# Kernel tuning notes

Measured on AMD Instinct MI355X. Metric: run time of the kernel, lower is better.

## Reference

```python
import jax, jax.numpy as jnp
import numpy as np

# ---- module hyperparameters (init_kwargs) ----
M = 6          # truncation level
D = 5          # path dimension
C = 4.0        # phi parameter
A = 1.0        # phi parameter a
SIGLEN = (D ** (M + 1) - 1) // (D - 1) - 1  # 19530
B, S = 64, 32  # batch x samples
N_BISECT = 100

# level id (1..M) of each signature coordinate: d^k coords at level k
LEVELS = jnp.asarray(np.repeat(np.arange(1, M + 1), [D ** k for k in range(1, M + 1)]), dtype=jnp.float32)  # [L]
# one-hot [L, M] mapping coordinates to their level, for per-level squared-norm sums
LEVEL_ONEHOT = jnp.asarray((np.repeat(np.arange(1, M + 1), [D ** k for k in range(1, M + 1)])[:, None] == np.arange(1, M + 1)[None, :]).astype(np.float32))


def setup_inputs() -> dict:
    key = jax.random.key(0)
    signatures = jax.random.normal(key, (B, S, SIGLEN), dtype=jnp.float32) * 0.5
    return {"signatures": signatures}


def _phi(x):
    # phi(x) = x for x <= C, else C + C^(1+a) (C^-a - x^-a)/a
    return jnp.where(x > C, C + C ** (1.0 + A) * (C ** (-A) - x ** (-A)) / A, x)


def _dilatation_norm(x):
    """x: [B,S,L] signatures. Returns norm lambda in [0,1], shape [B,S,1].
    Solves c0 + sum_k c_k t^{2k} = 0 on [0,2] by bisection (replaces brentq)."""
    x2 = x * x
    norm_quad = 1.0 + jnp.sum(x2, axis=-1)          # [B,S]
    c0 = 1.0 - _phi(norm_quad)                      # [B,S], <= 0
    ck = jnp.einsum('bsl,lm->bsm', x2, LEVEL_ONEHOT)  # [B,S,M] per-level squared norms
    coeffs = jnp.concatenate([c0[..., None], ck], axis=-1)  # [B,S,M+1]
    ks = jnp.arange(M + 1, dtype=jnp.float32)

    def poly(t):  # t: [B,S]
        return jnp.sum(coeffs * (t[..., None] ** 2) ** ks, axis=-1)

    def body(i, carry):
        lo, hi = carry
        mid = 0.5 * (lo + hi)
        neg = poly(mid) < 0.0
        return jnp.where(neg, mid, lo), jnp.where(neg, hi, mid)

    lo = jnp.zeros_like(c0)
    hi = jnp.full_like(c0, 2.0)
    lo, hi = jax.lax.fori_loop(0, N_BISECT, body, (lo, hi))
    root = 0.5 * (lo + hi)
    root = jnp.where(jnp.all(jnp.isfinite(coeffs), axis=-1), root, 0.0)
    root = jnp.minimum(root, 1.0)  # clamp as in dilatation()
    return root[..., None]          # [B,S,1]


def reference(signatures):
    # Normalization.apply + rescale + mean over samples (martingale_indices=None path)
    norm = _dilatation_norm(signatures)                       # [B,S,1]
    scaled = signatures * norm ** LEVELS[None, None, :]       # [B,S,L]
    return jnp.mean(scaled, axis=-2)                          # [B,L]
```

## Files before the change

kernel.cpp:

```cpp
#include <hip/hip_runtime.h>
#include <math.h>

#define BATCH   64
#define SAMP    32
#define SIGLEN  19530
#define NROWS   (BATCH * SAMP)
#define NF2     (SIGLEN / 2)
#define NBISECT 40


__device__ __forceinline__ int level0(int l) {
    return (l >= 5) + (l >= 30) + (l >= 155) + (l >= 780) + (l >= 3905);
}

__global__ __launch_bounds__(256) void sums_bisect_kernel(
        const float* __restrict__ x, float* __restrict__ pw) {
    const int bs = blockIdx.x;
    const float* __restrict__ row = x + (size_t)bs * SIGLEN;
    const int t = threadIdx.x;

    float a1 = 0.f, a2 = 0.f, a3 = 0.f, a4 = 0.f, a5 = 0.f, a6 = 0.f;

    if (t < 5)                              { float v = row[t];      a1 += v * v; }
    if (t >= 5 && t < 30)                   { float v = row[t];      a2 += v * v; }
    if (t >= 30 && t < 155)                 { float v = row[t];      a3 += v * v; }
    for (int l = 155 + t; l < 780; l += 256){ float v = row[l];      a4 += v * v; }

    {
        const float2* p = (const float2*)(row + 780);
        #pragma unroll 2
        for (int j = t; j < 1562; j += 256) { float2 v = p[j]; a5 += v.x * v.x + v.y * v.y; }
        if (t == 0) { float v = row[3904]; a5 += v * v; }
    }
    {
        if (t == 64) { float v = row[3905]; a6 += v * v; }
        const float2* p = (const float2*)(row + 3906);
        #pragma unroll 4
        for (int j = t; j < 7812; j += 256) { float2 v = p[j]; a6 += v.x * v.x + v.y * v.y; }
    }

    #pragma unroll
    for (int off = 32; off > 0; off >>= 1) {
        a1 += __shfl_xor(a1, off);
        a2 += __shfl_xor(a2, off);
        a3 += __shfl_xor(a3, off);
        a4 += __shfl_xor(a4, off);
        a5 += __shfl_xor(a5, off);
        a6 += __shfl_xor(a6, off);
    }

    __shared__ float red[4][6];
    const int wave = t >> 6, lane = t & 63;
    if (lane == 0) {
        red[wave][0] = a1; red[wave][1] = a2; red[wave][2] = a3;
        red[wave][3] = a4; red[wave][4] = a5; red[wave][5] = a6;
    }
    __syncthreads();

    if (t == 0) {
        float s1 = 0.f, s2 = 0.f, s3 = 0.f, s4 = 0.f, s5 = 0.f, s6 = 0.f;
        #pragma unroll
        for (int w = 0; w < 4; ++w) {
            s1 += red[w][0]; s2 += red[w][1]; s3 += red[w][2];
            s4 += red[w][3]; s5 += red[w][4]; s6 += red[w][5];
        }
        const float total = s1 + s2 + s3 + s4 + s5 + s6;
        const float nq = 1.0f + total;
        const float phi = (nq > 4.0f) ? (8.0f - 16.0f / nq) : nq;
        const float c0 = 1.0f - phi;
        const bool fin = isfinite(c0) && isfinite(total);

        float lo = 0.0f, hi = 2.0f;
        #pragma unroll 4
        for (int i = 0; i < NBISECT; ++i) {
            const float mid = 0.5f * (lo + hi);
            const float u = mid * mid;
            const float p = ((((((s6 * u + s5) * u + s4) * u + s3) * u + s2) * u + s1) * u) + c0;
            const bool neg = p < 0.0f;
            lo = neg ? mid : lo;
            hi = neg ? hi : mid;
        }
        float root = 0.5f * (lo + hi);
        if (!fin) root = 0.0f;
        root = fminf(root, 1.0f);

        float* dst = pw + (size_t)bs * 6;
        const float inv = 1.0f / SAMP;
        float w1 = root;
        float w2 = w1 * root, w3 = w2 * root, w4 = w3 * root, w5 = w4 * root, w6 = w5 * root;
        dst[0] = w1 * inv; dst[1] = w2 * inv; dst[2] = w3 * inv;
        dst[3] = w4 * inv; dst[4] = w5 * inv; dst[5] = w6 * inv;
    }
}

__global__ __launch_bounds__(256) void scale_mean_kernel(
        const float* __restrict__ x, const float* __restrict__ pw,
        float* __restrict__ out) {
    const int b = blockIdx.y;
    const int t = threadIdx.x;

    __shared__ float w[SAMP * 6];
    if (t < SAMP * 6) w[t] = pw[(size_t)b * (SAMP * 6) + t];
    __syncthreads();

    const int j = blockIdx.x * 256 + t;
    if (j >= NF2) return;

    const int l0 = 2 * j;
    const int levA = level0(l0);
    const int levB = level0(l0 + 1);

    const float2* __restrict__ x2p = (const float2*)x;
    const unsigned base = (unsigned)b * (SAMP * NF2) + (unsigned)j;

    float acc0 = 0.f, acc1 = 0.f;
    if (levA == levB) {
        #pragma unroll
        for (int s = 0; s < SAMP; ++s) {
            const float  ws = w[s * 6 + levA];
            const float2 v  = x2p[base + (unsigned)s * NF2];
            acc0 += v.x * ws;
            acc1 += v.y * ws;
        }
    } else {
        #pragma unroll
        for (int s = 0; s < SAMP; ++s) {
            const float2 v = x2p[base + (unsigned)s * NF2];
            acc0 += v.x * w[s * 6 + levA];
            acc1 += v.y * w[s * 6 + levB];
        }
    }

    float2 r; r.x = acc0; r.y = acc1;
    ((float2*)out)[(unsigned)b * NF2 + (unsigned)j] = r;
}

extern "C" void kernel_launch(void* const* d_in, const int* in_sizes, int n_in,
                              void* d_out, int out_size, void* d_ws, size_t ws_size,
                              hipStream_t stream) {
    const float* x = (const float*)d_in[0];
    float* out = (float*)d_out;
    float* pw = (float*)d_ws;

    sums_bisect_kernel<<<NROWS, 256, 0, stream>>>(x, pw);

    dim3 gridB((NF2 + 255) / 256, BATCH);
    scale_mean_kernel<<<gridB, 256, 0, stream>>>(x, pw, out);
}
```

Before: 254.0 us.

## Fuse norm and scale-mean into persistent cooperative kernel with per-batch flags

```diff
diff --git a/kernel.cpp b/kernel.cpp
--- a/kernel.cpp
+++ b/kernel.cpp
@@ -1,5 +1,8 @@
 #include <hip/hip_runtime.h>
+#include <hip/hip_cooperative_groups.h>
 #include <math.h>
+
+namespace cg = cooperative_groups;
 
 #define BATCH   64
 #define SAMP    32
@@ -7,49 +10,55 @@
 #define NROWS   (BATCH * SAMP)
 #define NF2     (SIGLEN / 2)
 #define NBISECT 40
-
+#define CHB     39
+#define NCHUNK  (BATCH * CHB)
+#define MAXBLK  1024
+
+
+__device__ float g_pw[NROWS * 6];
+__device__ int   g_done[BATCH];
 
 __device__ __forceinline__ int level0(int l) {
     return (l >= 5) + (l >= 30) + (l >= 155) + (l >= 780) + (l >= 3905);
 }
 
-__global__ __launch_bounds__(256) void sums_bisect_kernel(
-        const float* __restrict__ x, float* __restrict__ pw) {
-    const int bs = blockIdx.x;
-    const float* __restrict__ row = x + (size_t)bs * SIGLEN;
-    const int t = threadIdx.x;
-
+__device__ __forceinline__ void phase1_row(const float* __restrict__ x, int r, int t,
+                                           float (*red)[6]) {
+    const float* __restrict__ row = x + (size_t)r * SIGLEN;
     float a1 = 0.f, a2 = 0.f, a3 = 0.f, a4 = 0.f, a5 = 0.f, a6 = 0.f;
 
-    if (t < 5)                              { float v = row[t];      a1 += v * v; }
-    if (t >= 5 && t < 30)                   { float v = row[t];      a2 += v * v; }
-    if (t >= 30 && t < 155)                 { float v = row[t];      a3 += v * v; }
-    for (int l = 155 + t; l < 780; l += 256){ float v = row[l];      a4 += v * v; }
-
-    {
-        const float2* p = (const float2*)(row + 780);
-        #pragma unroll 2
-        for (int j = t; j < 1562; j += 256) { float2 v = p[j]; a5 += v.x * v.x + v.y * v.y; }
-        if (t == 0) { float v = row[3904]; a5 += v * v; }
-    }
-    {
-        if (t == 64) { float v = row[3905]; a6 += v * v; }
-        const float2* p = (const float2*)(row + 3906);
-        #pragma unroll 4
-        for (int j = t; j < 7812; j += 256) { float2 v = p[j]; a6 += v.x * v.x + v.y * v.y; }
+    if (t < 5)            { float v = row[t]; a1 += v * v; }
+    else if (t < 30)      { float v = row[t]; a2 += v * v; }
+    else if (t < 155)     { float v = row[t]; a3 += v * v; }
+    for (int l = 155 + t; l < 780; l += 256) { float v = row[l]; a4 += v * v; }
+
+    const int head = (r & 1) ? 2 : 0;
+    if (head) { if (t == 0)  { float v0 = row[780],   v1 = row[781];   a5 += v0*v0 + v1*v1; } }
+    else      { if (t == 32) { float v0 = row[19528], v1 = row[19529]; a6 += v0*v0 + v1*v1; } }
+
+    const float4* __restrict__ p4 = (const float4*)(row + 780 + head);
+    const int lb = 780 + head;
+    #pragma unroll 4
+    for (int q = t; q < 4687; q += 256) {
+        const float4 v = p4[q];
+        const int l = lb + 4 * q;
+        const float s = v.x*v.x + v.y*v.y + v.z*v.z + v.w*v.w;
+        if (l >= 3905)      a6 += s;
+        else if (l <= 3901) a5 += s;
+        else {
+            ((l     >= 3905) ? a6 : a5) += v.x * v.x;
+            ((l + 1 >= 3905) ? a6 : a5) += v.y * v.y;
+            ((l + 2 >= 3905) ? a6 : a5) += v.z * v.z;
+            ((l + 3 >= 3905) ? a6 : a5) += v.w * v.w;
+        }
     }
 
     #pragma unroll
     for (int off = 32; off > 0; off >>= 1) {
-        a1 += __shfl_xor(a1, off);
-        a2 += __shfl_xor(a2, off);
-        a3 += __shfl_xor(a3, off);
-        a4 += __shfl_xor(a4, off);
-        a5 += __shfl_xor(a5, off);
-        a6 += __shfl_xor(a6, off);
-    }
-
-    __shared__ float red[4][6];
+        a1 += __shfl_xor(a1, off); a2 += __shfl_xor(a2, off);
+        a3 += __shfl_xor(a3, off); a4 += __shfl_xor(a4, off);
+        a5 += __shfl_xor(a5, off); a6 += __shfl_xor(a6, off);
+    }
     const int wave = t >> 6, lane = t & 63;
     if (lane == 0) {
         red[wave][0] = a1; red[wave][1] = a2; red[wave][2] = a3;
@@ -65,18 +74,18 @@
             s4 += red[w][3]; s5 += red[w][4]; s6 += red[w][5];
         }
         const float total = s1 + s2 + s3 + s4 + s5 + s6;
-        const float nq = 1.0f + total;
+        const float nq  = 1.0f + total;
         const float phi = (nq > 4.0f) ? (8.0f - 16.0f / nq) : nq;
-        const float c0 = 1.0f - phi;
-        const bool fin = isfinite(c0) && isfinite(total);
+        const float c0  = 1.0f - phi;
+        const bool  fin = isfinite(c0) && isfinite(total);
 
         float lo = 0.0f, hi = 2.0f;
         #pragma unroll 4
         for (int i = 0; i < NBISECT; ++i) {
             const float mid = 0.5f * (lo + hi);
             const float u = mid * mid;
-            const float p = ((((((s6 * u + s5) * u + s4) * u + s3) * u + s2) * u + s1) * u) + c0;
-            const bool neg = p < 0.0f;
+            const float pv = ((((((s6*u + s5)*u + s4)*u + s3)*u + s2)*u + s1)*u) + c0;
+            const bool neg = pv < 0.0f;
             lo = neg ? mid : lo;
             hi = neg ? hi : mid;
         }
@@ -84,55 +93,89 @@
         if (!fin) root = 0.0f;
         root = fminf(root, 1.0f);
 
-        float* dst = pw + (size_t)bs * 6;
         const float inv = 1.0f / SAMP;
-        float w1 = root;
-        float w2 = w1 * root, w3 = w2 * root, w4 = w3 * root, w5 = w4 * root, w6 = w5 * root;
-        dst[0] = w1 * inv; dst[1] = w2 * inv; dst[2] = w3 * inv;
-        dst[3] = w4 * inv; dst[4] = w5 * inv; dst[5] = w6 * inv;
-    }
-}
-
-__global__ __launch_bounds__(256) void scale_mean_kernel(
-        const float* __restrict__ x, const float* __restrict__ pw,
-        float* __restrict__ out) {
-    const int b = blockIdx.y;
-    const int t = threadIdx.x;
-
-    __shared__ float w[SAMP * 6];
-    if (t < SAMP * 6) w[t] = pw[(size_t)b * (SAMP * 6) + t];
-    __syncthreads();
-
-    const int j = blockIdx.x * 256 + t;
-    if (j >= NF2) return;
-
-    const int l0 = 2 * j;
-    const int levA = level0(l0);
-    const int levB = level0(l0 + 1);
-
-    const float2* __restrict__ x2p = (const float2*)x;
-    const unsigned base = (unsigned)b * (SAMP * NF2) + (unsigned)j;
-
-    float acc0 = 0.f, acc1 = 0.f;
-    if (levA == levB) {
-        #pragma unroll
-        for (int s = 0; s < SAMP; ++s) {
-            const float  ws = w[s * 6 + levA];
-            const float2 v  = x2p[base + (unsigned)s * NF2];
-            acc0 += v.x * ws;
-            acc1 += v.y * ws;
-        }
-    } else {
-        #pragma unroll
-        for (int s = 0; s < SAMP; ++s) {
-            const float2 v = x2p[base + (unsigned)s * NF2];
-            acc0 += v.x * w[s * 6 + levA];
-            acc1 += v.y * w[s * 6 + levB];
-        }
-    }
-
-    float2 r; r.x = acc0; r.y = acc1;
-    ((float2*)out)[(unsigned)b * NF2 + (unsigned)j] = r;
+        float w1 = root, w2 = w1*root, w3 = w2*root, w4 = w3*root, w5 = w4*root, w6 = w5*root;
+        float* dst = g_pw + (size_t)r * 6;
+        __hip_atomic_store(dst + 0, w1 * inv, __ATOMIC_RELAXED, __HIP_MEMORY_SCOPE_AGENT);
+        __hip_atomic_store(dst + 1, w2 * inv, __ATOMIC_RELAXED, __HIP_MEMORY_SCOPE_AGENT);
+        __hip_atomic_store(dst + 2, w3 * inv, __ATOMIC_RELAXED, __HIP_MEMORY_SCOPE_AGENT);
+        __hip_atomic_store(dst + 3, w4 * inv, __ATOMIC_RELAXED, __HIP_MEMORY_SCOPE_AGENT);
+        __hip_atomic_store(dst + 4, w5 * inv, __ATOMIC_RELAXED, __HIP_MEMORY_SCOPE_AGENT);
+        __hip_atomic_store(dst + 5, w6 * inv, __ATOMIC_RELAXED, __HIP_MEMORY_SCOPE_AGENT);
+        __hip_atomic_fetch_add(&g_done[r >> 5], 1, __ATOMIC_RELEASE, __HIP_MEMORY_SCOPE_AGENT);
+    }
+    __syncthreads();
+}
+
+__device__ __forceinline__ void phase2_chunk(const float* __restrict__ x,
+                                             float* __restrict__ out,
+                                             int c, int t, float* wsh, bool spin) {
+    const int b  = c / CHB;
+    const int jc = c - b * CHB;
+
+    if (spin && t == 0) {
+        while (__hip_atomic_load(&g_done[b], __ATOMIC_ACQUIRE, __HIP_MEMORY_SCOPE_AGENT) < SAMP)
+            __builtin_amdgcn_s_sleep(8);
+    }
+    __syncthreads();
+    if (t < SAMP * 6)
+        wsh[t] = __hip_atomic_load(&g_pw[(size_t)b * (SAMP * 6) + t],
+                                   __ATOMIC_RELAXED, __HIP_MEMORY_SCOPE_AGENT);
+    __syncthreads();
+
+    const int j = jc * 256 + t;
+    if (j < NF2) {
+        const int l0 = 2 * j;
+        const int levA = level0(l0);
+        const int levB = level0(l0 + 1);
+        const float2* __restrict__ x2p = (const float2*)x;
+        const unsigned base = (unsigned)b * (SAMP * NF2) + (unsigned)j;
+
+        float acc0 = 0.f, acc1 = 0.f;
+        if (levA == levB) {
+            #pragma unroll
+            for (int s = 0; s < SAMP; ++s) {
+                const float  ws = wsh[s * 6 + levA];
+                const float2 v  = x2p[base + (unsigned)s * NF2];
+                acc0 += v.x * ws; acc1 += v.y * ws;
+            }
+        } else {
+            #pragma unroll
+            for (int s = 0; s < SAMP; ++s) {
+                const float2 v = x2p[base + (unsigned)s * NF2];
+                acc0 += v.x * wsh[s * 6 + levA];
+                acc1 += v.y * wsh[s * 6 + levB];
+            }
+        }
+        float2 rv; rv.x = acc0; rv.y = acc1;
+        ((float2*)out)[(unsigned)b * NF2 + (unsigned)j] = rv;
+    }
+}
+
+__global__ __launch_bounds__(256, 4) void es_fused_persistent(
+        const float* __restrict__ x, float* __restrict__ out) {
+    __shared__ float red[4][6];
+    __shared__ float wsh[SAMP * 6];
+    const int blk = blockIdx.x, nblk = gridDim.x, t = threadIdx.x;
+
+    if (blk == 0 && t < BATCH)
+        __hip_atomic_store(&g_done[t], 0, __ATOMIC_RELAXED, __HIP_MEMORY_SCOPE_AGENT);
+    cg::this_grid().sync();
+
+    for (int r = blk; r < NROWS; r += nblk)
+        phase1_row(x, r, t, red);
+    for (int c = blk; c < NCHUNK; c += nblk)
+        phase2_chunk(x, out, c, t, wsh, true);
+}
+
+__global__ __launch_bounds__(256) void es_phase1_kernel(const float* __restrict__ x) {
+    __shared__ float red[4][6];
+    phase1_row(x, blockIdx.x, threadIdx.x, red);
+}
+__global__ __launch_bounds__(256) void es_phase2_kernel(const float* __restrict__ x,
+                                                        float* __restrict__ out) {
+    __shared__ float wsh[SAMP * 6];
+    phase2_chunk(x, out, blockIdx.x, threadIdx.x, wsh, false);
 }
 
 extern "C" void kernel_launch(void* const* d_in, const int* in_sizes, int n_in,
@@ -140,10 +183,25 @@
                               hipStream_t stream) {
     const float* x = (const float*)d_in[0];
     float* out = (float*)d_out;
-    float* pw = (float*)d_ws;
-
-    sums_bisect_kernel<<<NROWS, 256, 0, stream>>>(x, pw);
-
-    dim3 gridB((NF2 + 255) / 256, BATCH);
-    scale_mean_kernel<<<gridB, 256, 0, stream>>>(x, pw, out);
-}
+    (void)d_ws; (void)ws_size;
+
+    static int nblk = -1;
+    if (nblk < 0) {
+        int mb = 0;
+        hipError_t e = hipOccupancyMaxActiveBlocksPerMultiprocessor(
+            &mb, (const void*)es_fused_persistent, 256, 0);
+        if (e != hipSuccess || mb < 1) mb = 0;
+        long cap = (long)mb * 256;
+        nblk = (int)(cap > MAXBLK ? MAXBLK : cap);
+    }
+
+    if (nblk > 0) {
+        void* args[] = { (void*)&x, (void*)&out };
+        if (hipLaunchCooperativeKernel((const void*)es_fused_persistent,
+                                       dim3(nblk), dim3(256), args, 0, stream) == hipSuccess)
+            return;
+        nblk = 0;
+    }
+    es_phase1_kernel<<<NROWS, 256, 0, stream>>>(x);
+    es_phase2_kernel<<<NCHUNK, 256, 0, stream>>>(x, out);
+}
```

New measurement: 379.0 us. 49.2% more time.
